# Kernel optimization log

Hardware: AMD Instinct MI355X
Metric: run time of the kernel (lower is better)

The kernel has to match this reference:

```python
import jax, jax.numpy as jnp
import numpy as np

NUM_LAYERS = 8
REL_SIZE = 16      # heads per layer
KEY_SIZE = 64
HIDDEN = REL_SIZE * KEY_SIZE  # 1024


def _mass_sincos(node_mass):
    # Sinusoidal embedding of scalar mass -> [B, N, 1, KEY_SIZE]
    half = KEY_SIZE // 2
    inv_freq = jnp.exp(-jnp.log(jnp.float32(10000.0)) * jnp.arange(half, dtype=jnp.float32) / half)
    ang = node_mass[..., None, None] * inv_freq  # [B, N, 1, half]
    return jnp.sin(ang), jnp.cos(ang)


def setup_inputs() -> dict:
    key = jax.random.key(0)
    k1, k2, k3, k4 = jax.random.split(key, 4)
    B, N = 4, 2048
    out_dim = HIDDEN * NUM_LAYERS * 2  # 16384
    node = jax.random.normal(k1, (B, N, HIDDEN), dtype=jnp.float32)
    node_mass = jax.random.uniform(k2, (B, N), dtype=jnp.float32) * 100.0
    W = jax.random.normal(k3, (HIDDEN, out_dim), dtype=jnp.float32) * (1.0 / np.sqrt(HIDDEN))
    b = jax.random.normal(k4, (out_dim,), dtype=jnp.float32) * 0.02
    return {"node": node, "node_mass": node_mass, "W": W, "b": b}


def reference(node, node_mass, W, b):
    B, N, _ = node.shape
    H = REL_SIZE * NUM_LAYERS  # heads per cache (k or v)
    # Fused KV projection: [B, N, 2*H, KEY_SIZE]
    kv = (jnp.einsum('bnh,ho->bno', node, W) + b).reshape(B, N, 2 * H, KEY_SIZE)
    k_cache, v_cache = kv[:, :, :H, :], kv[:, :, H:, :]
    # Rotary-style rotation of k_cache by mass sin/cos (broadcast over heads)
    dis_sin, dis_cos = _mass_sincos(node_mass)      # each [B, N, 1, KEY_SIZE//2]
    half = KEY_SIZE // 2
    x0, x1 = k_cache[..., :half], k_cache[..., half:]
    k_cache = jnp.concatenate([x0 * dis_cos - x1 * dis_sin,
                               x0 * dis_sin + x1 * dis_cos], axis=-1)
    # transpose(1, 2): [B, H, N, KEY_SIZE]; per-layer chunks are contiguous slices
    k_out = jnp.swapaxes(k_cache, 1, 2)
    v_out = jnp.swapaxes(v_cache, 1, 2)
    # Stack K and V caches; layer chunks = slices of size REL_SIZE along head dim
    return jnp.stack([k_out, v_out], axis=0)  # [2, B, H, N, KEY_SIZE]
```

## Files before the change

kernel.cpp:

```cpp
#include <hip/hip_runtime.h>
#include <stdint.h>

#define M_TOT 8192
#define N_TOT 16384
#define K_TOT 1024

typedef __bf16 bf16x8 __attribute__((ext_vector_type(8)));
typedef float f32x4 __attribute__((ext_vector_type(4)));

__device__ __forceinline__ unsigned short f2bf(float f) {
  unsigned int u = __float_as_uint(f);
  u = u + 0x7FFFu + ((u >> 16) & 1u);
  return (unsigned short)(u >> 16);
}

__device__ __forceinline__ void gload_lds16(const void* g, void* l) {
  __builtin_amdgcn_global_load_lds(
      (const __attribute__((address_space(1))) unsigned int*)g,
      (__attribute__((address_space(3))) unsigned int*)l,
      16, 0, 0);
}

__global__ __launch_bounds__(256) void k_convert_node(
    const float* __restrict__ src, unsigned short* __restrict__ dst) {
  size_t i0 = ((size_t)blockIdx.x * 256 + threadIdx.x) * 8;
#pragma unroll
  for (int it = 0; it < 2; it++) {
    size_t i = i0 + (size_t)it * (2048 * 256 * 8);
    f32x4 v0 = __builtin_nontemporal_load((const f32x4*)(src + i));
    f32x4 v1 = __builtin_nontemporal_load((const f32x4*)(src + i + 4));
    union { unsigned short u[8]; uint4 q; } r;
    r.u[0] = f2bf(v0[0]); r.u[1] = f2bf(v0[1]); r.u[2] = f2bf(v0[2]); r.u[3] = f2bf(v0[3]);
    r.u[4] = f2bf(v1[0]); r.u[5] = f2bf(v1[1]); r.u[6] = f2bf(v1[2]); r.u[7] = f2bf(v1[3]);
    *(uint4*)(dst + i) = r.q;
  }
}

__global__ __launch_bounds__(256) void k_transpose_w(
    const float* __restrict__ W, unsigned short* __restrict__ Wt) {
  __shared__ float tileT[64][68];
  int o0 = blockIdx.x * 64;
  int k0 = blockIdx.y * 64;
  int t = threadIdx.x;
  int kr0 = t >> 4, c4 = t & 15;
#pragma unroll
  for (int i = 0; i < 4; i++) {
    int kr = kr0 + i * 16;
    f32x4 v = __builtin_nontemporal_load(
        (const f32x4*)&W[(size_t)(k0 + kr) * N_TOT + o0 + c4 * 4]);
    tileT[c4 * 4 + 0][kr] = v[0];
    tileT[c4 * 4 + 1][kr] = v[1];
    tileT[c4 * 4 + 2][kr] = v[2];
    tileT[c4 * 4 + 3][kr] = v[3];
  }
  __syncthreads();
  int or0 = t >> 3, c8 = t & 7;
#pragma unroll
  for (int i = 0; i < 2; i++) {
    int orr = or0 + i * 32;
    float4 a = *(const float4*)&tileT[orr][c8 * 8];
    float4 b = *(const float4*)&tileT[orr][c8 * 8 + 4];
    union { unsigned short u[8]; uint4 q; } r;
    r.u[0] = f2bf(a.x); r.u[1] = f2bf(a.y); r.u[2] = f2bf(a.z); r.u[3] = f2bf(a.w);
    r.u[4] = f2bf(b.x); r.u[5] = f2bf(b.y); r.u[6] = f2bf(b.z); r.u[7] = f2bf(b.w);
    *(uint4*)&Wt[(size_t)(o0 + orr) * K_TOT + k0 + c8 * 8] = r.q;
  }
}

__global__ __launch_bounds__(256) void k_sincos(
    const float* __restrict__ mass, float* __restrict__ sin_t, float* __restrict__ cos_t) {
  int t = blockIdx.x * 256 + threadIdx.x;
  int row = t >> 5;
  int d = t & 31;
  float m = mass[row];
  float invf = expf(-0.28782313662425575f * (float)d);
  float ang = m * invf;
  float s, c;
  sincosf(ang, &s, &c);
  sin_t[t] = s;
  cos_t[t] = c;
}

__global__ __launch_bounds__(512, 4) void k_gemm256b(
    const unsigned short* __restrict__ A,
    const unsigned short* __restrict__ Bt,
    const float* __restrict__ bias,
    const float* __restrict__ sin_t,
    const float* __restrict__ cos_t,
    float* __restrict__ out)
{
  extern __shared__ char smem[];

  int tid  = threadIdx.x;
  int lane = tid & 63;
  int wid  = tid >> 6;
  int wm   = wid >> 1;
  int wn   = wid & 1;

  int orig = blockIdx.x;
  int x   = orig & 7;
  int c   = orig >> 3;
  int st  = c >> 5;
  int w   = c & 31;
  int bm0 = (x * 4 + (w >> 3)) * 256;
  int bn0 = (st * 8 + (w & 7)) * 128;

  int sv   = (tid & 7) ^ ((tid >> 3) & 7);
  int arow = ((tid >> 3) << 1) + (sv >> 2);
  int kst  = sv & 3;
  const unsigned short* srcA = A  + (size_t)(bm0 + arow) * K_TOT + kst * 8;
  const unsigned short* srcB = Bt + (size_t)(bn0 + arow) * K_TOT + kst * 8;

  int wofs = wid * 1024;

#define STAGE_A(s_, bo_) do { char* dA = smem + (bo_) + wofs; \
    const unsigned short* sa = srcA + (size_t)(s_) * 32; \
    gload_lds16(sa,                        dA); \
    gload_lds16(sa + (size_t)128 * K_TOT,  dA + 8192); } while (0)
#define STAGE_B(s_, bo_) do { char* dB = smem + (bo_) + 16384 + wofs; \
    gload_lds16(srcB + (size_t)(s_) * 32, dB); } while (0)

  STAGE_A(0, 0); STAGE_B(0, 0);
  STAGE_A(1, 24576); STAGE_B(1, 24576);

  f32x4 acc[4][4] = {};

  int r = lane & 15;
  int q = lane >> 4;
  int sl   = (((r & 1) << 2) + q) ^ ((r >> 1) & 7);
  int aoff = wm * 4096 + (r >> 1) * 128 + sl * 16;
  int boff = wn * 4096 + (r >> 1) * 128 + sl * 16;

  int cur = 0;
  int stg = 49152;

  for (int s = 0; s < 32; ++s) {
    if (s < 31) { asm volatile("s_waitcnt vmcnt(3)" ::: "memory"); }
    else        { asm volatile("s_waitcnt vmcnt(0)" ::: "memory"); }
    __builtin_amdgcn_s_barrier();
    __builtin_amdgcn_sched_barrier(0);

    const char* As_ = smem + cur;
    const char* Bs_ = As_ + 16384;

    bf16x8 bfrag[4], afrag[4];
#pragma unroll
    for (int ni = 0; ni < 4; ni++) bfrag[ni] = *(const bf16x8*)(Bs_ + boff + ni * 1024);
#pragma unroll
    for (int mi = 0; mi < 4; mi++) afrag[mi] = *(const bf16x8*)(As_ + aoff + mi * 1024);
    if (s < 30) { STAGE_A(s + 2, stg); STAGE_B(s + 2, stg); }
    __builtin_amdgcn_sched_barrier(0);
    __builtin_amdgcn_s_barrier();
    asm volatile("s_waitcnt lgkmcnt(0)" ::: "memory");
    __builtin_amdgcn_sched_barrier(0);
    __builtin_amdgcn_s_setprio(1);
#pragma unroll
    for (int mi = 0; mi < 4; mi++)
#pragma unroll
      for (int ni = 0; ni < 4; ni++)
        acc[mi][ni] = __builtin_amdgcn_mfma_f32_16x16x32_bf16(afrag[mi], bfrag[ni], acc[mi][ni], 0, 0, 0);
    __builtin_amdgcn_s_setprio(0);

    stg = cur;
    cur = (cur == 49152) ? 0 : cur + 24576;
  }
#undef STAGE_A
#undef STAGE_B

  int col16 = r;
  float bv[4];
#pragma unroll
  for (int ni = 0; ni < 4; ni++) bv[ni] = bias[bn0 + wn * 64 + ni * 16 + col16];

  int cgrp = (bn0 >> 6) + wn;
  int is_k = (cgrp < 128);
  int h = cgrp & 127;
  size_t sec = is_k ? 0 : 4;

#pragma unroll
  for (int mi = 0; mi < 4; mi++) {
#pragma unroll
    for (int reg = 0; reg < 4; reg++) {
      int row = bm0 + wm * 64 + mi * 16 + q * 4 + reg;
      int bb = row >> 11;
      int n  = row & 2047;
      float* op = out + (((sec + bb) * 128 + h) * 2048 + (size_t)n) * 64;
      if (is_k) {
#pragma unroll
        for (int ni = 0; ni < 2; ni++) {
          int d = ni * 16 + col16;
          float x0 = acc[mi][ni][reg]     + bv[ni];
          float x1 = acc[mi][ni + 2][reg] + bv[ni + 2];
          float sv2 = sin_t[row * 32 + d];
          float cv2 = cos_t[row * 32 + d];
          __builtin_nontemporal_store(x0 * cv2 - x1 * sv2, op + d);
          __builtin_nontemporal_store(x0 * sv2 + x1 * cv2, op + d + 32);
        }
      } else {
#pragma unroll
        for (int ni = 0; ni < 4; ni++) {
          int d = ni * 16 + col16;
          __builtin_nontemporal_store(acc[mi][ni][reg] + bv[ni], op + d);
        }
      }
    }
  }
}

extern "C" void kernel_launch(void* const* d_in, const int* in_sizes, int n_in,
                              void* d_out, int out_size, void* d_ws, size_t ws_size,
                              hipStream_t stream) {
  const float* node = (const float*)d_in[0];
  const float* mass = (const float*)d_in[1];
  const float* W    = (const float*)d_in[2];
  const float* bias = (const float*)d_in[3];
  float* out = (float*)d_out;

  const size_t NODE_B  = (size_t)M_TOT * K_TOT * 2;
  const size_t WT_B    = (size_t)N_TOT * K_TOT * 2;
  const size_t SIN_B   = (size_t)M_TOT * 32 * 4;
  if (ws_size < NODE_B + WT_B + 2 * SIN_B) return;

  char* ws = (char*)d_ws;
  unsigned short* nodeB = (unsigned short*)ws;
  unsigned short* WtB   = (unsigned short*)(ws + NODE_B);
  float* sin_t = (float*)(ws + NODE_B + WT_B);
  float* cos_t = (float*)(ws + NODE_B + WT_B + SIN_B);

  (void)hipFuncSetAttribute((const void*)k_gemm256b,
                            hipFuncAttributeMaxDynamicSharedMemorySize, 73728);

  k_convert_node<<<2048, 256, 0, stream>>>(node, nodeB);
  k_transpose_w<<<dim3(N_TOT / 64, K_TOT / 64), 256, 0, stream>>>(W, WtB);
  k_sincos<<<(M_TOT * 32) / 256, 256, 0, stream>>>(mass, sin_t, cos_t);
  k_gemm256b<<<dim3((M_TOT / 256) * (N_TOT / 128)), dim3(512), 73728, stream>>>(
      nodeB, WtB, bias, sin_t, cos_t, out);
}
```

Before: 331.8 us.

## Switch GEMM to 32x32x16 MFMA with 4 waves and larger per-wave tiles

Each block now runs 4 waves of 256 threads instead of 8, and each wave computes a 128x64 tile using 32x32x16 bf16 MFMA instead of 16x16x32. The LDS staging issues more loads per thread (4 for A, 2 for B), and the fragment loads and epilogue row and column mapping are adjusted to the 32x32 accumulator layout. The goal is fewer LDS fragment reads per FLOP and denser MFMA issue. The cost is higher register pressure (launch bounds 256,2) and fewer waves available to hide latency.

```diff
diff --git a/kernel.cpp b/kernel.cpp
--- a/kernel.cpp
+++ b/kernel.cpp
@@ -7,6 +7,7 @@
 
 typedef __bf16 bf16x8 __attribute__((ext_vector_type(8)));
 typedef float f32x4 __attribute__((ext_vector_type(4)));
+typedef float f32x16 __attribute__((ext_vector_type(16)));
 
 __device__ __forceinline__ unsigned short f2bf(float f) {
   unsigned int u = __float_as_uint(f);
@@ -81,7 +82,7 @@
   cos_t[t] = c;
 }
 
-__global__ __launch_bounds__(512, 4) void k_gemm256b(
+__global__ __launch_bounds__(256, 2) void k_gemm256b(
     const unsigned short* __restrict__ A,
     const unsigned short* __restrict__ Bt,
     const float* __restrict__ bias,
@@ -110,32 +111,37 @@
   int kst  = sv & 3;
   const unsigned short* srcA = A  + (size_t)(bm0 + arow) * K_TOT + kst * 8;
   const unsigned short* srcB = Bt + (size_t)(bn0 + arow) * K_TOT + kst * 8;
+  const size_t rs64 = (size_t)64 * K_TOT;
 
   int wofs = wid * 1024;
 
 #define STAGE_A(s_, bo_) do { char* dA = smem + (bo_) + wofs; \
     const unsigned short* sa = srcA + (size_t)(s_) * 32; \
-    gload_lds16(sa,                        dA); \
-    gload_lds16(sa + (size_t)128 * K_TOT,  dA + 8192); } while (0)
+    gload_lds16(sa,            dA); \
+    gload_lds16(sa + rs64,     dA + 4096); \
+    gload_lds16(sa + 2 * rs64, dA + 8192); \
+    gload_lds16(sa + 3 * rs64, dA + 12288); } while (0)
 #define STAGE_B(s_, bo_) do { char* dB = smem + (bo_) + 16384 + wofs; \
-    gload_lds16(srcB + (size_t)(s_) * 32, dB); } while (0)
+    const unsigned short* sb = srcB + (size_t)(s_) * 32; \
+    gload_lds16(sb,        dB); \
+    gload_lds16(sb + rs64, dB + 4096); } while (0)
 
   STAGE_A(0, 0); STAGE_B(0, 0);
   STAGE_A(1, 24576); STAGE_B(1, 24576);
 
-  f32x4 acc[4][4] = {};
-
-  int r = lane & 15;
-  int q = lane >> 4;
-  int sl   = (((r & 1) << 2) + q) ^ ((r >> 1) & 7);
-  int aoff = wm * 4096 + (r >> 1) * 128 + sl * 16;
-  int boff = wn * 4096 + (r >> 1) * 128 + sl * 16;
+  f32x16 acc[4][2] = {};
+
+  int r32 = lane & 31;
+  int hk  = lane >> 5;
+  int srow = r32 >> 1;
+  int sxor = srow & 7;
+  int rodd4 = (r32 & 1) << 2;
 
   int cur = 0;
   int stg = 49152;
 
   for (int s = 0; s < 32; ++s) {
-    if (s < 31) { asm volatile("s_waitcnt vmcnt(3)" ::: "memory"); }
+    if (s < 31) { asm volatile("s_waitcnt vmcnt(6)" ::: "memory"); }
     else        { asm volatile("s_waitcnt vmcnt(0)" ::: "memory"); }
     __builtin_amdgcn_s_barrier();
     __builtin_amdgcn_sched_barrier(0);
@@ -143,11 +149,19 @@
     const char* As_ = smem + cur;
     const char* Bs_ = As_ + 16384;
 
-    bf16x8 bfrag[4], afrag[4];
-#pragma unroll
-    for (int ni = 0; ni < 4; ni++) bfrag[ni] = *(const bf16x8*)(Bs_ + boff + ni * 1024);
-#pragma unroll
-    for (int mi = 0; mi < 4; mi++) afrag[mi] = *(const bf16x8*)(As_ + aoff + mi * 1024);
+    bf16x8 aF[4][2], bF[2][2];
+#pragma unroll
+    for (int mi = 0; mi < 4; mi++)
+#pragma unroll
+      for (int kk = 0; kk < 2; kk++)
+        aF[mi][kk] = *(const bf16x8*)(As_ + wm * 8192 + mi * 2048 + srow * 128
+                                      + (((rodd4 + kk * 2 + hk) ^ sxor) << 4));
+#pragma unroll
+    for (int ni = 0; ni < 2; ni++)
+#pragma unroll
+      for (int kk = 0; kk < 2; kk++)
+        bF[ni][kk] = *(const bf16x8*)(Bs_ + wn * 4096 + ni * 2048 + srow * 128
+                                      + (((rodd4 + kk * 2 + hk) ^ sxor) << 4));
     if (s < 30) { STAGE_A(s + 2, stg); STAGE_B(s + 2, stg); }
     __builtin_amdgcn_sched_barrier(0);
     __builtin_amdgcn_s_barrier();
@@ -155,10 +169,13 @@
     __builtin_amdgcn_sched_barrier(0);
     __builtin_amdgcn_s_setprio(1);
 #pragma unroll
-    for (int mi = 0; mi < 4; mi++)
-#pragma unroll
-      for (int ni = 0; ni < 4; ni++)
-        acc[mi][ni] = __builtin_amdgcn_mfma_f32_16x16x32_bf16(afrag[mi], bfrag[ni], acc[mi][ni], 0, 0, 0);
+    for (int kk = 0; kk < 2; kk++)
+#pragma unroll
+      for (int mi = 0; mi < 4; mi++)
+#pragma unroll
+        for (int ni = 0; ni < 2; ni++)
+          acc[mi][ni] = __builtin_amdgcn_mfma_f32_32x32x16_bf16(
+              aF[mi][kk], bF[ni][kk], acc[mi][ni], 0, 0, 0);
     __builtin_amdgcn_s_setprio(0);
 
     stg = cur;
@@ -167,10 +184,8 @@
 #undef STAGE_A
 #undef STAGE_B
 
-  int col16 = r;
-  float bv[4];
-#pragma unroll
-  for (int ni = 0; ni < 4; ni++) bv[ni] = bias[bn0 + wn * 64 + ni * 16 + col16];
+  float bv0 = bias[bn0 + wn * 64 + r32];
+  float bv1 = bias[bn0 + wn * 64 + 32 + r32];
 
   int cgrp = (bn0 >> 6) + wn;
   int is_k = (cgrp < 128);
@@ -180,28 +195,21 @@
 #pragma unroll
   for (int mi = 0; mi < 4; mi++) {
 #pragma unroll
-    for (int reg = 0; reg < 4; reg++) {
-      int row = bm0 + wm * 64 + mi * 16 + q * 4 + reg;
+    for (int j = 0; j < 16; j++) {
+      int row = bm0 + wm * 128 + mi * 32 + (j & 3) + ((j >> 2) << 3) + (hk << 2);
       int bb = row >> 11;
       int n  = row & 2047;
       float* op = out + (((sec + bb) * 128 + h) * 2048 + (size_t)n) * 64;
       if (is_k) {
-#pragma unroll
-        for (int ni = 0; ni < 2; ni++) {
-          int d = ni * 16 + col16;
-          float x0 = acc[mi][ni][reg]     + bv[ni];
-          float x1 = acc[mi][ni + 2][reg] + bv[ni + 2];
-          float sv2 = sin_t[row * 32 + d];
-          float cv2 = cos_t[row * 32 + d];
-          __builtin_nontemporal_store(x0 * cv2 - x1 * sv2, op + d);
-          __builtin_nontemporal_store(x0 * sv2 + x1 * cv2, op + d + 32);
-        }
+        float x0 = acc[mi][0][j] + bv0;
+        float x1 = acc[mi][1][j] + bv1;
+        float sv2 = sin_t[row * 32 + r32];
+        float cv2 = cos_t[row * 32 + r32];
+        __builtin_nontemporal_store(x0 * cv2 - x1 * sv2, op + r32);
+        __builtin_nontemporal_store(x0 * sv2 + x1 * cv2, op + r32 + 32);
       } else {
-#pragma unroll
-        for (int ni = 0; ni < 4; ni++) {
-          int d = ni * 16 + col16;
-          __builtin_nontemporal_store(acc[mi][ni][reg] + bv[ni], op + d);
-        }
+        __builtin_nontemporal_store(acc[mi][0][j] + bv0, op + r32);
+        __builtin_nontemporal_store(acc[mi][1][j] + bv1, op + r32 + 32);
       }
     }
   }
@@ -233,6 +241,6 @@
   k_convert_node<<<2048, 256, 0, stream>>>(node, nodeB);
   k_transpose_w<<<dim3(N_TOT / 64, K_TOT / 64), 256, 0, stream>>>(W, WtB);
   k_sincos<<<(M_TOT * 32) / 256, 256, 0, stream>>>(mass, sin_t, cos_t);
-  k_gemm256b<<<dim3((M_TOT / 256) * (N_TOT / 128)), dim3(512), 73728, stream>>>(
+  k_gemm256b<<<dim3((M_TOT / 256) * (N_TOT / 128)), dim3(256), 73728, stream>>>(
       nodeB, WtB, bias, sin_t, cos_t, out);
 }
```

Result: slower. 391.5 us (+18.0%).
